# Kernel tuning notes

Hardware: AMD Instinct MI355X
Metric: run time of the kernel (lower is better)

The kernel has to match this reference:

```python
import jax, jax.numpy as jnp
import numpy as np

B, T, F = 256, 64, 32
ENC_U = 256
DEC_U = 2 * ENC_U   # must equal 2*enc_units (Dense W2 built on enc_hidden first)
VOCAB = 2048
EMB = DEC_U         # embedding_dim = decoder_units
EPS = 1e-3          # keras BatchNormalization default epsilon


def setup_inputs() -> dict:
    key = jax.random.key(0)
    ks = jax.random.split(key, 16)
    def n(k, shape, s=0.05):
        return jax.random.normal(k, shape, jnp.float32) * s
    z = lambda *s: jnp.zeros(s, jnp.float32)
    return {
        "enc_input": jax.random.normal(ks[0], (B, T, F), jnp.float32),
        "bn_e_gamma": jnp.ones((F,), jnp.float32),
        "bn_e_beta": z(F),
        "Wx_f": n(ks[1], (F, 3 * ENC_U)), "Wh_f": n(ks[2], (ENC_U, 3 * ENC_U)),
        "bx_f": z(3 * ENC_U), "bh_f": z(3 * ENC_U),
        "Wx_b": n(ks[3], (F, 3 * ENC_U)), "Wh_b": n(ks[4], (ENC_U, 3 * ENC_U)),
        "bx_b": z(3 * ENC_U), "bh_b": z(3 * ENC_U),
        "W1": n(ks[5], (2 * ENC_U, DEC_U)), "b1": z(DEC_U),
        "W2": n(ks[6], (DEC_U, DEC_U)), "b2": z(DEC_U),
        "V": n(ks[7], (DEC_U, 1)), "bV": z(1),
        "emb": n(ks[8], (VOCAB, EMB)),
        "bn_d_gamma": jnp.ones((2 * ENC_U + EMB,), jnp.float32),
        "bn_d_beta": z(2 * ENC_U + EMB),
        "Wx_d": n(ks[9], (2 * ENC_U + EMB, 3 * DEC_U)), "Wh_d": n(ks[10], (DEC_U, 3 * DEC_U)),
        "bx_d": z(3 * DEC_U), "bh_d": z(3 * DEC_U),
        "Wfc": n(ks[11], (DEC_U, VOCAB)), "bfc": z(VOCAB),
        "targ": jax.random.randint(ks[12], (B, T), 0, VOCAB),
    }


def _run_gru(x_proj, h0, Wh, bh):
    """Keras GRU (reset_after=True, gate order z,r,n). x_proj: [B,T,3U]."""
    def step(h, xp):
        hp = h @ Wh + bh
        xz, xr, xh = jnp.split(xp, 3, axis=-1)
        hz, hr, hn = jnp.split(hp, 3, axis=-1)
        zg = jax.nn.sigmoid(xz + hz)
        rg = jax.nn.sigmoid(xr + hr)
        ng = jnp.tanh(xh + rg * hn)
        h_new = zg * h + (1.0 - zg) * ng
        return h_new, h_new
    hT, outs = jax.lax.scan(step, h0, jnp.swapaxes(x_proj, 0, 1))
    return jnp.swapaxes(outs, 0, 1), hT


def _forward(enc_input, bn_e_gamma, bn_e_beta, Wx_f, Wh_f, bx_f, bh_f,
             Wx_b, Wh_b, bx_b, bh_b, W1, b1, W2, b2, V, bV, emb,
             bn_d_gamma, bn_d_beta, Wx_d, Wh_d, bx_d, bh_d, Wfc, bfc, targ):
    # Encoder: BN (inference: mean=0, var=1) -> bidirectional GRU
    xn = enc_input * (bn_e_gamma / jnp.sqrt(1.0 + EPS)) + bn_e_beta
    h0 = jnp.zeros((xn.shape[0], ENC_U), xn.dtype)
    out_f, hf = _run_gru(xn @ Wx_f + bx_f, h0, Wh_f, bh_f)
    out_br, hb = _run_gru(xn[:, ::-1] @ Wx_b + bx_b, h0, Wh_b, bh_b)
    enc_out = jnp.concatenate([out_f, out_br[:, ::-1]], axis=-1)  # [B,T,2U]
    dec_h0 = jnp.concatenate([hf, hb], axis=-1)                   # [B,2U]

    keys = enc_out @ W1 + b1            # attention keys, constant over steps
    emb_t = emb[targ]                   # [B,T,EMB] teacher-forced inputs
    g_d = bn_d_gamma / jnp.sqrt(1.0 + EPS)

    def dec_step(h, e):
        # Bahdanau attention with query = previous step's GRU state
        q = h @ W2 + b2                                           # [B,A]
        score = jnp.squeeze(jnp.tanh(keys + q[:, None, :]) @ V, -1) + bV  # [B,T]
        w = jax.nn.softmax(score, axis=1)
        ctx = jnp.einsum('bt,btu->bu', w, enc_out)                # [B,2U]
        x = jnp.concatenate([ctx, e], axis=-1) * g_d + bn_d_beta  # BN inference
        # decoder GRU: called WITHOUT initial_state in original -> h_prev = 0
        xp = x @ Wx_d + bx_d
        xz, xr, xh = jnp.split(xp, 3, axis=-1)
        hz, hr, hn = jnp.split(bh_d, 3, axis=-1)  # h_prev @ Wh_d == 0
        zg = jax.nn.sigmoid(xz + hz)
        rg = jax.nn.sigmoid(xr + hr)
        ng = jnp.tanh(xh + rg * hn)
        h_new = (1.0 - zg) * ng                   # zg * h_prev == 0
        return h_new, h_new @ Wfc + bfc

    _, logits = jax.lax.scan(jax.checkpoint(dec_step), dec_h0,
                             jnp.swapaxes(emb_t, 0, 1))
    return jnp.swapaxes(logits, 0, 1)  # [B,T,VOCAB]


def reference(enc_input, bn_e_gamma, bn_e_beta, Wx_f, Wh_f, bx_f, bh_f,
              Wx_b, Wh_b, bx_b, bh_b, W1, b1, W2, b2, V, bV, emb,
              bn_d_gamma, bn_d_beta, Wx_d, Wh_d, bx_d, bh_d, Wfc, bfc, targ):
    return _forward(enc_input, bn_e_gamma, bn_e_beta, Wx_f, Wh_f, bx_f, bh_f,
                    Wx_b, Wh_b, bx_b, bh_b, W1, b1, W2, b2, V, bV, emb,
                    bn_d_gamma, bn_d_beta, Wx_d, Wh_d, bx_d, bh_d, Wfc, bfc, targ)
```

## Files before the change

### kernel.cpp

```cpp
#include <hip/hip_runtime.h>

static constexpr float INV_SQ = 0.99950037468777319f;

typedef __attribute__((ext_vector_type(8))) unsigned short us8;
typedef __attribute__((ext_vector_type(2))) unsigned short us2;
typedef __attribute__((ext_vector_type(8))) _Float16 f16x8;
typedef __attribute__((ext_vector_type(2))) _Float16 f16x2;
typedef __attribute__((ext_vector_type(4))) float f32x4;

__device__ __forceinline__ float h2f(unsigned short u) {
    union { unsigned short q; _Float16 h; } cv; cv.q = u; return (float)cv.h;
}
__device__ __forceinline__ unsigned short f2h(float x) {
    union { _Float16 h; unsigned short u; } cv; cv.h = (_Float16)x; return cv.u;
}
__device__ __forceinline__ float sigm(float x) { return 1.0f / (1.0f + __expf(-x)); }
__device__ __forceinline__ float fdot2f(f16x2 a, f16x2 b, float c) {
#if __has_builtin(__builtin_amdgcn_fdot2)
    return __builtin_amdgcn_fdot2(a, b, c, false);
#else
    return c + (float)a[0] * (float)b[0] + (float)a[1] * (float)b[1];
#endif
}

__global__ __launch_bounds__(512)
void repack_enc(float* __restrict__ out,
                const float* __restrict__ WhF, const float* __restrict__ WhB,
                const float* __restrict__ WxF, const float* __restrict__ WxB)
{
    unsigned short* up = (unsigned short*)out;
    const int id = blockIdx.x * 512 + threadIdx.x;
    if (id < 393216) {
        const int dir = (id >= 196608) ? 1 : 0;
        const int r = id - dir * 196608;
        const int u = r / 768;
        const int rr = r - u * 768;
        const int g = rr >> 8, upp = rr & 255;
        const float v = (dir ? WhB : WhF)[upp * 768 + g * 256 + u];
        up[(size_t)(11520 + (id >> 10)) * 4096 + 2560 + (id & 1023)] = f2h(v);
    } else if (id < 442368) {
        const int x = id - 393216;
        const int dir = (x >= 24576) ? 1 : 0;
        const int r = x - dir * 24576;
        const int g = r >> 13;
        const int r2 = r & 8191;
        const int fp = r2 >> 9;
        const int r3 = r2 & 511;
        const int u = r3 >> 1, j = r3 & 1;
        const float v = (dir ? WxB : WxF)[(fp * 2 + j) * 768 + g * 256 + u];
        up[(size_t)(11904 + (x >> 10)) * 4096 + 2560 + (x & 1023)] = f2h(v);
    }
}

__global__ __launch_bounds__(768, 1)
void enc_gru(const float* __restrict__ x,
             const float* __restrict__ g_e, const float* __restrict__ b_e,
             const float* __restrict__ bxF, const float* __restrict__ bhF,
             const float* __restrict__ bxB, const float* __restrict__ bhB,
             float* __restrict__ out)
{
    const int tid = threadIdx.x;
    const int dir = blockIdx.x & 1;
    const int b0  = (blockIdx.x >> 1) * 2;
    const int u = tid & 255, g = tid >> 8;

    const float* bx = dir ? bxB : bxF;
    const float* bh = dir ? bhB : bhF;

    __shared__ us2 WxL[12288];
    __shared__ __align__(16) unsigned short hsH[2][256];
    __shared__ float hsF[2][256];
    __shared__ float part[4][2][256];
    __shared__ __align__(16) unsigned short xsH[2][32];

    const unsigned short* u16p = (const unsigned short*)out;

    for (int i = 0; i < 16; ++i) {
        const int fi = dir * 24576 + (tid * 16 + i) * 2;
        const size_t a = (size_t)(11904 + (fi >> 10)) * 4096 + 2560 + (fi & 1023);
        WxL[tid * 16 + i] = *reinterpret_cast<const us2*>(u16p + a);
    }
    us8 ebw[32];
    {
        const int base = dir * 196608 + (u * 3 + g) * 256;
        #pragma unroll
        for (int k = 0; k < 32; ++k) {
            const int fi = base + k * 8;
            const size_t a = (size_t)(11520 + (fi >> 10)) * 4096 + 2560 + (fi & 1023);
            ebw[k] = *reinterpret_cast<const us8*>(u16p + a);
        }
    }
    if (tid < 256) {
        hsF[0][tid] = 0.0f; hsF[1][tid] = 0.0f;
        hsH[0][tid] = 0;    hsH[1][tid] = 0;
    }
    const float bxg = bx[g * 256 + u], bhg = bh[g * 256 + u];
    __syncthreads();

    for (int t = 0; t < 64; ++t) {
        const int ts = dir ? (63 - t) : t;
        if (tid < 64) {
            const int f = tid & 31, bs = tid >> 5;
            xsH[bs][f] = f2h(x[((b0 + bs) * 64 + ts) * 32 + f] * (g_e[f] * INV_SQ) + b_e[f]);
        }
        __syncthreads();

        float ax0 = bxg, ax1 = bxg, ah0 = bhg, ah1 = bhg;
        {
            const us2* xs0 = reinterpret_cast<const us2*>(&xsH[0][0]);
            const us2* xs1 = reinterpret_cast<const us2*>(&xsH[1][0]);
            #pragma unroll
            for (int fp = 0; fp < 16; ++fp) {
                union { us2 q; f16x2 h; } w, a0, a1;
                w.q = WxL[(g * 16 + fp) * 256 + u];
                a0.q = xs0[fp]; a1.q = xs1[fp];
                ax0 = fdot2f(w.h, a0.h, ax0);
                ax1 = fdot2f(w.h, a1.h, ax1);
            }
        }
        #pragma unroll
        for (int k = 0; k < 32; ++k) {
            union { us8 q; f16x2 p[4]; } w, h0, h1;
            w.q = ebw[k];
            h0.q = *reinterpret_cast<const us8*>(&hsH[0][k * 8]);
            h1.q = *reinterpret_cast<const us8*>(&hsH[1][k * 8]);
            #pragma unroll
            for (int j = 0; j < 4; ++j) {
                ah0 = fdot2f(w.p[j], h0.p[j], ah0);
                ah1 = fdot2f(w.p[j], h1.p[j], ah1);
            }
        }
        if (g < 2) {
            part[g][0][u] = ax0 + ah0;
            part[g][1][u] = ax1 + ah1;
        } else {
            part[2][0][u] = ax0; part[2][1][u] = ax1;
            part[3][0][u] = ah0; part[3][1][u] = ah1;
        }
        __syncthreads();
        if (tid < 512) {
            const int bs = tid >> 8, uu = tid & 255;
            const float z = sigm(part[0][bs][uu]);
            const float r = sigm(part[1][bs][uu]);
            const float n = tanhf(part[2][bs][uu] + r * part[3][bs][uu]);
            const float hp = hsF[bs][uu];
            const float h = z * hp + (1.0f - z) * n;
            hsF[bs][uu] = h;
            hsH[bs][uu] = f2h(h);
            out[((b0 + bs) * 64 + ts) * 2048 + dir * 256 + uu] = h;
        }
        __syncthreads();
    }
}

__global__ __launch_bounds__(256)
void embx_k(float* __restrict__ out, const float* __restrict__ emb,
            const float* __restrict__ g, const float* __restrict__ be,
            const float* __restrict__ Wxd, const float* __restrict__ bxd)
{
    __shared__ __align__(16) float As[16 * 512];
    const int tid = threadIdx.x;
    const int r0  = blockIdx.x * 16;
    const int n0  = blockIdx.y * 512;

    #pragma unroll
    for (int i = 0; i < 32; ++i) {
        const int idx = tid + i * 256;
        const int r = idx >> 9, k = idx & 511;
        As[idx] = emb[(r0 + r) * 512 + k] * (g[512 + k] * INV_SQ) + be[512 + k];
    }
    __syncthreads();

    const int n1 = n0 + tid, n2 = n0 + tid + 256;
    float cv1 = bxd[n1], cv2 = bxd[n2];
    for (int i = 0; i < 512; ++i) {
        const float bi = be[i];
        cv1 += bi * Wxd[i * 1536 + n1];
        cv2 += bi * Wxd[i * 1536 + n2];
    }

    float acc1[16], acc2[16];
    #pragma unroll
    for (int r = 0; r < 16; ++r) { acc1[r] = cv1; acc2[r] = cv2; }

    for (int k = 0; k < 512; k += 4) {
        float w1[4], w2[4];
        #pragma unroll
        for (int kk = 0; kk < 4; ++kk) {
            w1[kk] = Wxd[(512 + k + kk) * 1536 + n1];
            w2[kk] = Wxd[(512 + k + kk) * 1536 + n2];
        }
        #pragma unroll
        for (int r = 0; r < 16; ++r) {
            const float4 a = *reinterpret_cast<const float4*>(&As[r * 512 + k]);
            acc1[r] += a.x * w1[0] + a.y * w1[1] + a.z * w1[2] + a.w * w1[3];
            acc2[r] += a.x * w2[0] + a.y * w2[1] + a.z * w2[2] + a.w * w2[3];
        }
    }

    unsigned short* up = (unsigned short*)out;
    #pragma unroll
    for (int r = 0; r < 16; ++r) {
        const size_t base = (size_t)(8192 + r0 + r) * 4096 + 2560;
        up[base + n1] = f2h(acc1[r]);
        up[base + n2] = f2h(acc2[r]);
    }
}

__global__ __launch_bounds__(512)
void repack_k(float* __restrict__ out, const float* __restrict__ W2,
              const float* __restrict__ Wxd, const float* __restrict__ W1,
              const float* __restrict__ g1)
{
    unsigned short* up = (unsigned short*)out;
    const int id = blockIdx.x * 512 + threadIdx.x;
    if (id < 262144) {
        const int k8 = id >> 12, rem = id & 4095, c = rem >> 3, j = rem & 7;
        up[(size_t)(10240 + (id >> 10)) * 4096 + 2560 + (id & 1023)] =
            f2h(W2[(k8 * 8 + j) * 512 + c]);
    } else if (id < 1048576) {
        const int x = id - 262144;
        const int n = x >> 9, k = x & 511;
        up[(size_t)(10496 + (x >> 10)) * 4096 + 2560 + (x & 1023)] =
            f2h(Wxd[k * 1536 + n] * (g1[k] * INV_SQ));
    } else {
        const int x = id - 1048576;
        const int n = x >> 9, k = x & 511;
        up[(size_t)(11264 + (x >> 10)) * 4096 + 2560 + (x & 1023)] =
            f2h(W1[k * 512 + n]);
    }
}

template <int MODE>
__global__ __launch_bounds__(256, 2)
void gemm64(float* __restrict__ out, const float* __restrict__ bias)
{
    constexpr int NT   = (MODE == 0) ? 24 : 8;
    constexpr int BROW = (MODE == 0) ? 10496 : 11264;
    const int tid = threadIdx.x;
    const int wid = tid >> 6, lane = tid & 63;
    const int row16 = lane & 15, kg = lane >> 4;
    const int m0 = blockIdx.x * 64;
    const unsigned short* u16p = (const unsigned short*)out;
    unsigned short* up = (unsigned short*)out;

    __shared__ __align__(16) char aL[65536];

    for (int i = tid; i < 8192; i += 256) {
        const int m = i >> 7, k4 = (i & 127) << 2;
        const float4 v = *reinterpret_cast<const float4*>(out + (size_t)(m0 + m) * 2048 + k4);
        union { unsigned long long u64; _Float16 h[4]; } p;
        p.h[0] = (_Float16)v.x; p.h[1] = (_Float16)v.y;
        p.h[2] = (_Float16)v.z; p.h[3] = (_Float16)v.w;
        const int off = (m * 1024 + k4 * 2) ^ ((m & 7) << 4);
        *reinterpret_cast<unsigned long long*>(aL + off) = p.u64;
    }
    __syncthreads();

    for (int i = 0; i < NT / 4; ++i) {
        const int nt = i * 4 + wid;
        const int n0t = nt * 64;
        f32x4 acc[4][4];
        #pragma unroll
        for (int mi = 0; mi < 4; ++mi)
            #pragma unroll
            for (int ni = 0; ni < 4; ++ni) {
                f32x4 z = {0.f, 0.f, 0.f, 0.f};
                acc[mi][ni] = z;
            }
        size_t bb[4];
        #pragma unroll
        for (int ni = 0; ni < 4; ++ni) {
            const int n = n0t + ni * 16 + row16;
            bb[ni] = (size_t)(BROW + (n >> 1)) * 4096 + 2560 + (n & 1) * 512 + kg * 8;
        }
        #pragma unroll 2
        for (int k0 = 0; k0 < 512; k0 += 32) {
            f16x8 af[4], bfr[4];
            #pragma unroll
            for (int mi = 0; mi < 4; ++mi) {
                const int row = mi * 16 + row16;
                const int off = (row * 1024 + (k0 + kg * 8) * 2) ^ ((row & 7) << 4);
                af[mi] = *reinterpret_cast<const f16x8*>(aL + off);
            }
            #pragma unroll
            for (int ni = 0; ni < 4; ++ni)
                bfr[ni] = *reinterpret_cast<const f16x8*>(u16p + bb[ni] + k0);
            #pragma unroll
            for (int mi = 0; mi < 4; ++mi)
                #pragma unroll
                for (int ni = 0; ni < 4; ++ni)
                    acc[mi][ni] = __builtin_amdgcn_mfma_f32_16x16x32_f16(
                        af[mi], bfr[ni], acc[mi][ni], 0, 0, 0);
        }
        #pragma unroll
        for (int mi = 0; mi < 4; ++mi) {
            #pragma unroll
            for (int ni = 0; ni < 4; ++ni) {
                const int n = n0t + ni * 16 + row16;
                if constexpr (MODE == 0) {
                    #pragma unroll
                    for (int r = 0; r < 4; ++r)
                        up[(size_t)(m0 + mi * 16 + kg * 4 + r) * 4096 + 1024 + n] =
                            f2h(acc[mi][ni][r]);
                } else {
                    const float bv = bias[n];
                    #pragma unroll
                    for (int r = 0; r < 4; ++r) {
                        const int ttm = mi * 16 + kg * 4 + r;
                        up[(size_t)(blockIdx.x * 32 + (n >> 4)) * 4096 + 2560 +
                           ((n & 15) << 6) + ttm] = f2h(acc[mi][ni][r] + bv);
                    }
                }
            }
        }
    }
}

__global__ __launch_bounds__(512, 1)
void decoder(float* __restrict__ out,
             const float* __restrict__ b2,
             const float* __restrict__ V, const float* __restrict__ bV,
             const float* __restrict__ bh_d, const int* __restrict__ targ)
{
    const int b = blockIdx.x, tid = threadIdx.x;
    __shared__ __align__(16) unsigned short keysL[32768];
    __shared__ __align__(16) unsigned short hsH[512];
    __shared__ float qs[512], Vl[512];
    __shared__ float part[8][64], wv[64];
    __shared__ float xpP[2][1536];
    __shared__ int   tokL[64];

    float* erow = out + (size_t)b * 131072;
    const unsigned short* u16p = (const unsigned short*)out;

    #pragma unroll
    for (int i8 = tid * 8; i8 < 32768; i8 += 4096)
        *reinterpret_cast<us8*>(&keysL[i8]) =
            *reinterpret_cast<const us8*>(u16p + (size_t)(b * 32 + (i8 >> 10)) * 4096
                                          + 2560 + (i8 & 1023));

    hsH[tid] = f2h((tid < 256) ? erow[63 * 2048 + tid] : erow[tid]);
    Vl[tid] = V[tid];
    if (tid < 64) tokL[tid] = targ[b * 64 + tid];
    const float b2c = b2[tid];
    const float bhz = bh_d[tid], bhr = bh_d[512 + tid], bhn = bh_d[1024 + tid];
    const float bVv = bV[0];
    const int lo7 = tid & 127, hi3 = tid >> 7;
    const size_t w2base = (size_t)(10240 + hi3) * 4096 + 2560 + lo7 * 8;

    const int jh = tid >> 8;
    const int ch = tid & 255;
    us2 ebv[96];
    {
        const size_t ebase = (size_t)(b * 64 + jh * 32) * 4096 + 1024 + ch * 6;
        #pragma unroll
        for (int r = 0; r < 32; ++r) {
            const unsigned short* p = u16p + ebase + (size_t)r * 4096;
            ebv[r * 3 + 0] = *reinterpret_cast<const us2*>(p);
            ebv[r * 3 + 1] = *reinterpret_cast<const us2*>(p + 2);
            ebv[r * 3 + 2] = *reinterpret_cast<const us2*>(p + 4);
        }
    }
    __syncthreads();

    for (int t = 0; t < 64; ++t) {
        const int tok = tokL[t];
        const size_t eb = (size_t)(8192 + tok) * 4096 + 2560;
        const unsigned short exz = u16p[eb + tid];
        const unsigned short exr = u16p[eb + 512 + tid];
        const unsigned short exh = u16p[eb + 1024 + tid];
        {
            float a0 = 0.0f, a1 = 0.0f;
            #pragma unroll 4
            for (int k8 = 0; k8 < 64; k8 += 2) {
                union { us8 u; f16x2 p[4]; } w0, w1, h0, h1;
                w0.u = *reinterpret_cast<const us8*>(u16p + w2base + (size_t)k8 * 16384);
                w1.u = *reinterpret_cast<const us8*>(u16p + w2base + (size_t)(k8 + 1) * 16384);
                h0.u = *reinterpret_cast<const us8*>(&hsH[k8 * 8]);
                h1.u = *reinterpret_cast<const us8*>(&hsH[k8 * 8 + 8]);
                #pragma unroll
                for (int p = 0; p < 4; ++p) {
                    a0 = fdot2f(w0.p[p], h0.p[p], a0);
                    a1 = fdot2f(w1.p[p], h1.p[p], a1);
                }
            }
            qs[tid] = a0 + a1 + b2c;
        }
        __syncthreads();
        {
            const int tt = tid & 63, tq = tid >> 6;
            float p = 0.0f;
            #pragma unroll 4
            for (int n = tq * 64; n < tq * 64 + 64; ++n) {
                float xx = h2f(keysL[n * 64 + tt]) + qs[n];
                xx = fminf(fmaxf(xx, -20.0f), 20.0f);
                const float e = __expf(2.0f * xx);
                p += (e - 1.0f) / (e + 1.0f) * Vl[n];
            }
            part[tq][tt] = p;
        }
        __syncthreads();
        {
            const int L = tid & 63;
            float sc = bVv;
            #pragma unroll
            for (int q8 = 0; q8 < 8; ++q8) sc += part[q8][L];
            float m = sc;
            m = fmaxf(m, __shfl_xor(m, 1));
            m = fmaxf(m, __shfl_xor(m, 2));
            m = fmaxf(m, __shfl_xor(m, 4));
            m = fmaxf(m, __shfl_xor(m, 8));
            m = fmaxf(m, __shfl_xor(m, 16));
            m = fmaxf(m, __shfl_xor(m, 32));
            const float ev = __expf(sc - m);
            float s = ev;
            s += __shfl_xor(s, 1);
            s += __shfl_xor(s, 2);
            s += __shfl_xor(s, 4);
            s += __shfl_xor(s, 8);
            s += __shfl_xor(s, 16);
            s += __shfl_xor(s, 32);
            wv[L] = ev / s;
        }
        __syncthreads();
        {
            float a0 = 0, a1 = 0, a2 = 0, a3 = 0, a4 = 0, a5 = 0;
            const float* wvp = &wv[jh * 32];
            #pragma unroll
            for (int r = 0; r < 32; ++r) {
                const float w = wvp[r];
                const us2 e0 = ebv[r * 3 + 0];
                const us2 e1 = ebv[r * 3 + 1];
                const us2 e2 = ebv[r * 3 + 2];
                a0 += w * h2f(e0[0]); a1 += w * h2f(e0[1]);
                a2 += w * h2f(e1[0]); a3 += w * h2f(e1[1]);
                a4 += w * h2f(e2[0]); a5 += w * h2f(e2[1]);
            }
            float* xq = &xpP[jh][ch * 6];
            xq[0] = a0; xq[1] = a1; xq[2] = a2;
            xq[3] = a3; xq[4] = a4; xq[5] = a5;
        }
        __syncthreads();
        {
            const float xz = h2f(exz) + (xpP[0][tid]        + xpP[1][tid]);
            const float xr = h2f(exr) + (xpP[0][512 + tid]  + xpP[1][512 + tid]);
            const float xh = h2f(exh) + (xpP[0][1024 + tid] + xpP[1][1024 + tid]);
            const float z = sigm(xz + bhz), r = sigm(xr + bhr);
            const float h = (1.0f - z) * tanhf(xh + r * bhn);
            hsH[tid] = f2h(h);
            erow[t * 2048 + tid] = h;
        }
        __syncthreads();
    }
}

__global__ __launch_bounds__(256)
void logits_m(float* __restrict__ out, const float* __restrict__ Wfc,
              const float* __restrict__ bfc)
{
    const int tid = threadIdx.x;
    const int wid = tid >> 6, lane = tid & 63;
    const int row16 = lane & 15, kg = lane >> 4;
    const int m0 = blockIdx.x * 64;

    __shared__ __align__(16) char aL[65536];
    __shared__ __align__(16) char bL[65536];

    for (int i = tid; i < 8192; i += 256) {
        const int m = i >> 7, k4 = (i & 127) << 2;
        const float4 v = *reinterpret_cast<const float4*>(out + (size_t)(m0 + m) * 2048 + k4);
        union { unsigned long long u64; _Float16 h[4]; } p;
        p.h[0] = (_Float16)v.x; p.h[1] = (_Float16)v.y;
        p.h[2] = (_Float16)v.z; p.h[3] = (_Float16)v.w;
        const int off = (m * 1024 + k4 * 2) ^ ((m & 7) << 4);
        *reinterpret_cast<unsigned long long*>(aL + off) = p.u64;
    }

    for (int nt = 0; nt < 32; ++nt) {
        const int n0t = nt * 64;
        __syncthreads();
        for (int i = tid; i < 8192; i += 256) {
            const int k = i >> 4, n4 = (i & 15) << 2;
            const float4 v = *reinterpret_cast<const float4*>(Wfc + (size_t)k * 2048 + n0t + n4);
            const int k2 = k * 2;
            *reinterpret_cast<_Float16*>(bL + (((n4 + 0) * 1024 + k2) ^ (((n4 + 0) & 7) << 4))) = (_Float16)v.x;
            *reinterpret_cast<_Float16*>(bL + (((n4 + 1) * 1024 + k2) ^ (((n4 + 1) & 7) << 4))) = (_Float16)v.y;
            *reinterpret_cast<_Float16*>(bL + (((n4 + 2) * 1024 + k2) ^ (((n4 + 2) & 7) << 4))) = (_Float16)v.z;
            *reinterpret_cast<_Float16*>(bL + (((n4 + 3) * 1024 + k2) ^ (((n4 + 3) & 7) << 4))) = (_Float16)v.w;
        }
        __syncthreads();

        f32x4 acc[4];
        #pragma unroll
        for (int ni = 0; ni < 4; ++ni) {
            f32x4 z = {0.f, 0.f, 0.f, 0.f};
            acc[ni] = z;
        }
        #pragma unroll 2
        for (int k0 = 0; k0 < 512; k0 += 32) {
            const int row = wid * 16 + row16;
            const int aoff = (row * 1024 + (k0 + kg * 8) * 2) ^ ((row & 7) << 4);
            const f16x8 af = *reinterpret_cast<const f16x8*>(aL + aoff);
            #pragma unroll
            for (int ni = 0; ni < 4; ++ni) {
                const int nr = ni * 16 + row16;
                const int boff = (nr * 1024 + (k0 + kg * 8) * 2) ^ ((nr & 7) << 4);
                const f16x8 bf_ = *reinterpret_cast<const f16x8*>(bL + boff);
                acc[ni] = __builtin_amdgcn_mfma_f32_16x16x32_f16(af, bf_, acc[ni], 0, 0, 0);
            }
        }
        #pragma unroll
        for (int ni = 0; ni < 4; ++ni) {
            const int n = n0t + ni * 16 + row16;
            const float bv = bfc[n];
            #pragma unroll
            for (int r = 0; r < 4; ++r)
                out[(size_t)(m0 + wid * 16 + kg * 4 + r) * 2048 + n] = acc[ni][r] + bv;
        }
    }
}

extern "C" void kernel_launch(void* const* d_in, const int* in_sizes, int n_in,
                              void* d_out, int out_size, void* d_ws, size_t ws_size,
                              hipStream_t stream) {
    (void)in_sizes; (void)n_in; (void)out_size; (void)d_ws; (void)ws_size;
    const float* enc_input = (const float*)d_in[0];
    const float* bn_e_g    = (const float*)d_in[1];
    const float* bn_e_b    = (const float*)d_in[2];
    const float* Wx_f      = (const float*)d_in[3];
    const float* Wh_f      = (const float*)d_in[4];
    const float* bx_f      = (const float*)d_in[5];
    const float* bh_f      = (const float*)d_in[6];
    const float* Wx_b      = (const float*)d_in[7];
    const float* Wh_b      = (const float*)d_in[8];
    const float* bx_b      = (const float*)d_in[9];
    const float* bh_b      = (const float*)d_in[10];
    const float* W1        = (const float*)d_in[11];
    const float* b1        = (const float*)d_in[12];
    const float* W2        = (const float*)d_in[13];
    const float* b2        = (const float*)d_in[14];
    const float* V         = (const float*)d_in[15];
    const float* bV        = (const float*)d_in[16];
    const float* emb       = (const float*)d_in[17];
    const float* bn_d_g    = (const float*)d_in[18];
    const float* bn_d_b    = (const float*)d_in[19];
    const float* Wx_d      = (const float*)d_in[20];
    const float* bx_d      = (const float*)d_in[22];
    const float* bh_d      = (const float*)d_in[23];
    const float* Wfc       = (const float*)d_in[24];
    const float* bfc       = (const float*)d_in[25];
    const int*   targ      = (const int*)d_in[26];

    float* out = (float*)d_out;

    repack_enc<<<dim3(864), dim3(512), 0, stream>>>(out, Wh_f, Wh_b, Wx_f, Wx_b);
    enc_gru<<<dim3(256), dim3(768), 0, stream>>>(
        enc_input, bn_e_g, bn_e_b, bx_f, bh_f, bx_b, bh_b, out);
    embx_k<<<dim3(128, 3), dim3(256), 0, stream>>>(out, emb, bn_d_g, bn_d_b, Wx_d, bx_d);
    repack_k<<<dim3(2560), dim3(512), 0, stream>>>(out, W2, Wx_d, W1, bn_d_g);
    gemm64<2><<<dim3(256), dim3(256), 0, stream>>>(out, b1);
    gemm64<0><<<dim3(256), dim3(256), 0, stream>>>(out, b1);
    decoder<<<dim3(256), dim3(512), 0, stream>>>(out, b2, V, bV, bh_d, targ);
    logits_m<<<dim3(256), dim3(256), 0, stream>>>(out, Wfc, bfc);
}
```

Measured before the change: 2.094 ms.

## Keep attention keys in registers and rewrite tanh via exp2 and rcp

Pre-scales the attention keys by 2*log2(e) when the producer kernel writes them, and keeps each thread's 64 keys in float registers instead of a 64KB LDS array. The tanh·V sum is rewritten as a constant base plus a sum of -2V/(exp2(k+q)+1), using the hardware exp2 and reciprocal and dropping the clamp and divide. This removes LDS traffic and divisions from the per-step score loop. The cost is higher register pressure (64 extra floats per thread) and reduced precision and overflow handling from the approximate rcp without clamping.

Result: slower. 2.626 ms (+25.4%).

```diff
diff --git a/kernel.cpp b/kernel.cpp
--- a/kernel.cpp
+++ b/kernel.cpp
@@ -1,6 +1,7 @@
 #include <hip/hip_runtime.h>
 
 static constexpr float INV_SQ = 0.99950037468777319f;
+static constexpr float TLN2E  = 2.8853900817779268f;
 
 typedef __attribute__((ext_vector_type(8))) unsigned short us8;
 typedef __attribute__((ext_vector_type(2))) unsigned short us2;
@@ -20,6 +21,20 @@
     return __builtin_amdgcn_fdot2(a, b, c, false);
 #else
     return c + (float)a[0] * (float)b[0] + (float)a[1] * (float)b[1];
+#endif
+}
+__device__ __forceinline__ float aexp2(float x) {
+#if __has_builtin(__builtin_amdgcn_exp2f)
+    return __builtin_amdgcn_exp2f(x);
+#else
+    return exp2f(x);
+#endif
+}
+__device__ __forceinline__ float arcp(float x) {
+#if __has_builtin(__builtin_amdgcn_rcpf)
+    return __builtin_amdgcn_rcpf(x);
+#else
+    return 1.0f / x;
 #endif
 }
 
@@ -309,7 +324,7 @@
                     for (int r = 0; r < 4; ++r) {
                         const int ttm = mi * 16 + kg * 4 + r;
                         up[(size_t)(blockIdx.x * 32 + (n >> 4)) * 4096 + 2560 +
-                           ((n & 15) << 6) + ttm] = f2h(acc[mi][ni][r] + bv);
+                           ((n & 15) << 6) + ttm] = f2h((acc[mi][ni][r] + bv) * TLN2E);
                     }
                 }
             }
@@ -324,9 +339,8 @@
              const float* __restrict__ bh_d, const int* __restrict__ targ)
 {
     const int b = blockIdx.x, tid = threadIdx.x;
-    __shared__ __align__(16) unsigned short keysL[32768];
     __shared__ __align__(16) unsigned short hsH[512];
-    __shared__ float qs[512], Vl[512];
+    __shared__ float qs2[512], Vm2[512];
     __shared__ float part[8][64], wv[64];
     __shared__ float xpP[2][1536];
     __shared__ int   tokL[64];
@@ -334,14 +348,8 @@
     float* erow = out + (size_t)b * 131072;
     const unsigned short* u16p = (const unsigned short*)out;
 
-    #pragma unroll
-    for (int i8 = tid * 8; i8 < 32768; i8 += 4096)
-        *reinterpret_cast<us8*>(&keysL[i8]) =
-            *reinterpret_cast<const us8*>(u16p + (size_t)(b * 32 + (i8 >> 10)) * 4096
-                                          + 2560 + (i8 & 1023));
-
     hsH[tid] = f2h((tid < 256) ? erow[63 * 2048 + tid] : erow[tid]);
-    Vl[tid] = V[tid];
+    Vm2[tid] = -2.0f * V[tid];
     if (tid < 64) tokL[tid] = targ[b * 64 + tid];
     const float b2c = b2[tid];
     const float bhz = bh_d[tid], bhr = bh_d[512 + tid], bhn = bh_d[1024 + tid];
@@ -349,6 +357,15 @@
     const int lo7 = tid & 127, hi3 = tid >> 7;
     const size_t w2base = (size_t)(10240 + hi3) * 4096 + 2560 + lo7 * 8;
 
+    const int tt = tid & 63, tq = tid >> 6;
+    float kreg[64];
+    #pragma unroll
+    for (int i = 0; i < 64; ++i) {
+        const int n = tq * 64 + i;
+        kreg[i] = h2f(u16p[(size_t)(b * 32 + (n >> 4)) * 4096 + 2560
+                           + ((n & 15) << 6) + tt]);
+    }
+
     const int jh = tid >> 8;
     const int ch = tid & 255;
     us2 ebv[96];
@@ -363,6 +380,9 @@
         }
     }
     __syncthreads();
+    float pbase = 0.0f;
+    for (int i = 0; i < 64; ++i) pbase += Vm2[tq * 64 + i];
+    pbase *= -0.5f;
 
     for (int t = 0; t < 64; ++t) {
         const int tok = tokL[t];
@@ -385,18 +405,17 @@
                     a1 = fdot2f(w1.p[p], h1.p[p], a1);
                 }
             }
-            qs[tid] = a0 + a1 + b2c;
+            qs2[tid] = (a0 + a1 + b2c) * TLN2E;
         }
         __syncthreads();
         {
-            const int tt = tid & 63, tq = tid >> 6;
-            float p = 0.0f;
-            #pragma unroll 4
-            for (int n = tq * 64; n < tq * 64 + 64; ++n) {
-                float xx = h2f(keysL[n * 64 + tt]) + qs[n];
-                xx = fminf(fmaxf(xx, -20.0f), 20.0f);
-                const float e = __expf(2.0f * xx);
-                p += (e - 1.0f) / (e + 1.0f) * Vl[n];
+            float p = pbase;
+            #pragma unroll
+            for (int i = 0; i < 64; ++i) {
+                const int n = tq * 64 + i;
+                const float e = aexp2(kreg[i] + qs2[n]);
+                const float r = arcp(e + 1.0f);
+                p = fmaf(Vm2[n], r, p);
             }
             part[tq][tt] = p;
         }
```
